# Kernel optimization log

Measured on AMD Instinct MI355X. Metric: run time of the kernel, lower is better.

Reference implementation:

```python
import jax, jax.numpy as jnp
import numpy as np

CHUNK_SIZE = 1024  # module default chunk_size


def setup_inputs() -> dict:
    key = jax.random.key(0)
    kq, kk, kv = jax.random.split(key, 3)
    B, H, S, D = 2, 16, 2048, 64
    q = jax.random.normal(kq, (B, H, S, D), dtype=jnp.float32)
    k = jax.random.normal(kk, (B, H, S, D), dtype=jnp.float32)
    v = jax.random.normal(kv, (B, H, S, D), dtype=jnp.float32)
    return {"q": q, "k": k, "v": v}


def reference(q, k, v):
    # Chunked causal attention: q split into chunks of CHUNK_SIZE along seq,
    # each chunk attends to the full K/V with causal mask (tril, diagonal=start).
    B, H, S, D = q.shape
    scale = D ** (-0.5)
    cs = CHUNK_SIZE
    nc = S // cs  # S is a multiple of chunk_size here
    qc = q.reshape(B, H, nc, cs, D)
    # scores: [B, H, nc, cs, S]
    scores = jnp.einsum('bhncd,bhsd->bhncs', qc, k) * scale
    # causal mask per chunk: key position j visible iff j <= chunk_start + i
    row = (jnp.arange(nc) * cs)[:, None, None] + jnp.arange(cs)[None, :, None]  # [nc, cs, 1]
    col = jnp.arange(S)[None, None, :]  # [1, 1, S]
    causal = col <= row  # [nc, cs, S]
    scores = jnp.where(causal[None, None], scores, -jnp.inf)
    attn = jax.nn.softmax(scores, axis=-1)
    out = jnp.einsum('bhncs,bhsd->bhncd', attn, v)
    return out.reshape(B, H, S, D)
```

## Files before the change

### kernel.cpp

```cpp
#include <hip/hip_runtime.h>

typedef __bf16 bf16x8 __attribute__((ext_vector_type(8)));
typedef float f32x4 __attribute__((ext_vector_type(4)));

#define S_LEN 2048
#define D_DIM 64
#define NHEAD 32

typedef __attribute__((address_space(1))) const void gas;
typedef __attribute__((address_space(3))) void las;

__global__ __launch_bounds__(256) void convert_kv(const float* __restrict__ K,
                                                  const float* __restrict__ V,
                                                  __bf16* __restrict__ Kb,
                                                  __bf16* __restrict__ Vtg) {
    const int head = blockIdx.y;
    const int s0   = blockIdx.x * 64;
    const int tr   = threadIdx.x >> 2;
    const int tc   = (threadIdx.x & 3) << 4;
    const size_t ib = (size_t)head * (S_LEN * D_DIM) + (size_t)(s0 + tr) * D_DIM + tc;

    __shared__ __bf16 tb[64][72];

    {
        const float* kr = K + ib;
        f32x4 a = *(const f32x4*)kr, b = *(const f32x4*)(kr + 4),
              c = *(const f32x4*)(kr + 8), d = *(const f32x4*)(kr + 12);
        bf16x8 o0, o1;
        #pragma unroll
        for (int e = 0; e < 4; ++e) {
            o0[e] = (__bf16)a[e]; o0[e + 4] = (__bf16)b[e];
            o1[e] = (__bf16)c[e]; o1[e + 4] = (__bf16)d[e];
        }
        __bf16* ko = Kb + ib;
        *(bf16x8*)ko = o0; *(bf16x8*)(ko + 8) = o1;
    }
    {
        const float* vr = V + ib;
        f32x4 a = *(const f32x4*)vr, b = *(const f32x4*)(vr + 4),
              c = *(const f32x4*)(vr + 8), d = *(const f32x4*)(vr + 12);
        #pragma unroll
        for (int e = 0; e < 4; ++e) {
            tb[tc +  e][tr] = (__bf16)a[e];
            tb[tc + 4 + e][tr] = (__bf16)b[e];
            tb[tc + 8 + e][tr] = (__bf16)c[e];
            tb[tc + 12 + e][tr] = (__bf16)d[e];
        }
    }
    __syncthreads();
    {
        bf16x8 o0, o1;
        #pragma unroll
        for (int e = 0; e < 8; ++e) { o0[e] = tb[tr][tc + e]; o1[e] = tb[tr][tc + 8 + e]; }
        __bf16* vo = Vtg + (size_t)head * (D_DIM * S_LEN) + (size_t)tr * S_LEN + s0 + tc;
        *(bf16x8*)vo = o0; *(bf16x8*)(vo + 8) = o1;
    }
}

__global__ __launch_bounds__(256, 4) void attn_fwd(const float* __restrict__ Q,
                                                   const __bf16* __restrict__ Kb,
                                                   const __bf16* __restrict__ Vg,
                                                   float* __restrict__ O) {
    const int b    = blockIdx.x;
    const int xcd  = b & 7;
    const int cs   = (b >> 3) & 31;
    const int j    = b >> 8;
    const int head = xcd * 4 + (cs >> 3);
    const int slot = cs & 7;
    const int chunk = (j == 0) ? slot : (j == 1) ? (31 - slot)
                    : (j == 2) ? (slot + 8) : (23 - slot);

    const int tid  = threadIdx.x;
    const int wave = tid >> 6;
    const int lane = tid & 63;
    const int l15  = lane & 15;
    const int lhi  = lane >> 4;

    const int q0 = chunk * 64 + wave * 16;
    const size_t qbase = (size_t)head * (S_LEN * D_DIM);
    const size_t vbase = (size_t)head * (D_DIM * S_LEN);
    const float qscale = 0.125f * 1.44269504088896340736f;

    __shared__ __align__(16) __bf16 Klds[2][64][64];
    __shared__ __align__(16) __bf16 Vt[2][64][64];
    __shared__ __align__(16) __bf16 Plds[4][16][64];

    const int xsw = (lane & 7) ^ ((lane >> 3) & 7);
    const size_t kOff = (size_t)(lane >> 3) * D_DIM + (size_t)xsw * 8;
    const size_t vOff = (size_t)(lane >> 3) * S_LEN + (size_t)xsw * 8;
    const __bf16* kgw = Kb + qbase + (size_t)(wave * 16) * D_DIM + kOff;
    const __bf16* vgw = Vg + vbase + (size_t)(wave * 16) * S_LEN + vOff;

    bf16x8 qf[2];
    {
        const float* qrow = Q + qbase + (size_t)(q0 + l15) * D_DIM + lhi * 8;
        #pragma unroll
        for (int h = 0; h < 2; ++h) {
            f32x4 a = *(const f32x4*)(qrow + h * 32);
            f32x4 bq = *(const f32x4*)(qrow + h * 32 + 4);
            bf16x8 t;
            #pragma unroll
            for (int e = 0; e < 4; ++e) { t[e] = (__bf16)(a[e] * qscale); t[e + 4] = (__bf16)(bq[e] * qscale); }
            qf[h] = t;
        }
    }

    f32x4 acc[4];
    #pragma unroll
    for (int td = 0; td < 4; ++td) acc[td] = (f32x4){0.f, 0.f, 0.f, 0.f};
    float m_r = -1e30f, l_r = 0.f;

    auto stage = [&](int kv0, int bufi) {
        const __bf16* kg = kgw + (size_t)kv0 * D_DIM;
        const __bf16* vg = vgw + kv0;
        __builtin_amdgcn_global_load_lds((gas*)kg,                 (las*)&Klds[bufi][wave * 16][0],     16, 0, 0);
        __builtin_amdgcn_global_load_lds((gas*)(kg + 8 * D_DIM),   (las*)&Klds[bufi][wave * 16 + 8][0], 16, 0, 0);
        __builtin_amdgcn_global_load_lds((gas*)vg,                 (las*)&Vt[bufi][wave * 16][0],       16, 0, 0);
        __builtin_amdgcn_global_load_lds((gas*)(vg + 8 * S_LEN),   (las*)&Vt[bufi][wave * 16 + 8][0],   16, 0, 0);
    };

    stage(0, 0);

    const int nt = chunk + 1;
    for (int kt = 0; kt < nt; ++kt) {
        const int cur = kt & 1;
        asm volatile("s_waitcnt vmcnt(0)" ::: "memory");
        __syncthreads();

        if (kt + 1 < nt) stage((kt + 1) << 6, cur ^ 1);

        f32x4 s[4];
        #pragma unroll
        for (int ct = 0; ct < 4; ++ct) s[ct] = (f32x4){0.f, 0.f, 0.f, 0.f};
        __builtin_amdgcn_s_setprio(1);
        #pragma unroll
        for (int h = 0; h < 2; ++h) {
            #pragma unroll
            for (int ct = 0; ct < 4; ++ct) {
                const int krow = ct * 16 + l15;
                bf16x8 kf = *(const bf16x8*)&Klds[cur][krow][(h * 32 + lhi * 8) ^ ((l15 & 7) << 3)];
                s[ct] = __builtin_amdgcn_mfma_f32_16x16x32_bf16(kf, qf[h], s[ct], 0, 0, 0);
            }
        }
        __builtin_amdgcn_s_setprio(0);

        if (kt == nt - 1) {
            const int kv0 = kt << 6;
            const int qg = q0 + l15;
            #pragma unroll
            for (int ct = 0; ct < 4; ++ct)
                #pragma unroll
                for (int r = 0; r < 4; ++r) {
                    const int kg = kv0 + ct * 16 + lhi * 4 + r;
                    if (kg > qg) s[ct][r] = -1e30f;
                }
        }

        float mm = fmaxf(fmaxf(fmaxf(s[0][0], s[0][1]), fmaxf(s[0][2], s[0][3])),
                         fmaxf(fmaxf(s[1][0], s[1][1]), fmaxf(s[1][2], s[1][3])));
        mm = fmaxf(mm, fmaxf(fmaxf(fmaxf(s[2][0], s[2][1]), fmaxf(s[2][2], s[2][3])),
                             fmaxf(fmaxf(s[3][0], s[3][1]), fmaxf(s[3][2], s[3][3]))));
        mm = fmaxf(mm, __shfl_xor(mm, 16));
        mm = fmaxf(mm, __shfl_xor(mm, 32));
        if (!__all(mm - m_r <= 8.0f)) {
            const float mn = fmaxf(m_r, mm);
            const float f = exp2f(m_r - mn);
            m_r = mn;
            l_r *= f;
            #pragma unroll
            for (int r = 0; r < 4; ++r) {
                const float fr = __shfl(f, lhi * 4 + r);
                #pragma unroll
                for (int td = 0; td < 4; ++td) acc[td][r] *= fr;
            }
        }
        float ps = 0.f;
        #pragma unroll
        for (int ct = 0; ct < 4; ++ct)
            #pragma unroll
            for (int r = 0; r < 4; ++r) {
                const float p = exp2f(s[ct][r] - m_r);
                s[ct][r] = p;
                ps += p;
            }
        ps += __shfl_xor(ps, 16);
        ps += __shfl_xor(ps, 32);
        l_r += ps;

        #pragma unroll
        for (int ct = 0; ct < 4; ++ct) {
            union { __bf16 h[4]; unsigned long long u; } pw;
            #pragma unroll
            for (int r = 0; r < 4; ++r) pw.h[r] = (__bf16)s[ct][r];
            *(unsigned long long*)&Plds[wave][l15][(ct * 16 + lhi * 4) ^ ((l15 & 7) << 3)] = pw.u;
        }
        asm volatile("s_waitcnt lgkmcnt(0)" ::: "memory");
        bf16x8 pf[2];
        #pragma unroll
        for (int kh = 0; kh < 2; ++kh)
            pf[kh] = *(const bf16x8*)&Plds[wave][l15][(kh * 32 + lhi * 8) ^ ((l15 & 7) << 3)];
        asm volatile("" ::: "memory");

        __builtin_amdgcn_s_setprio(1);
        #pragma unroll
        for (int kh = 0; kh < 2; ++kh) {
            #pragma unroll
            for (int td = 0; td < 4; ++td) {
                const int vrow = td * 16 + l15;
                bf16x8 vf = *(const bf16x8*)&Vt[cur][vrow][(kh * 32 + lhi * 8) ^ ((vrow & 7) << 3)];
                acc[td] = __builtin_amdgcn_mfma_f32_16x16x32_bf16(pf[kh], vf, acc[td], 0, 0, 0);
            }
        }
        __builtin_amdgcn_s_setprio(0);
    }

    float* orow = O + qbase + (size_t)q0 * D_DIM;
    #pragma unroll
    for (int r = 0; r < 4; ++r) {
        const float inv = 1.0f / __shfl(l_r, lhi * 4 + r);
        #pragma unroll
        for (int td = 0; td < 4; ++td)
            orow[(size_t)(lhi * 4 + r) * D_DIM + td * 16 + l15] = acc[td][r] * inv;
    }
}

__global__ __launch_bounds__(256, 4) void attn_fwd_fb(const float* __restrict__ Q,
                                                      const float* __restrict__ K,
                                                      const float* __restrict__ V,
                                                      float* __restrict__ O) {
    const int b    = blockIdx.x;
    const int xcd  = b & 7;
    const int cs   = (b >> 3) & 31;
    const int j    = b >> 8;
    const int head = xcd * 4 + (cs >> 3);
    const int slot = cs & 7;
    const int chunk = (j == 0) ? slot : (j == 1) ? (31 - slot)
                    : (j == 2) ? (slot + 8) : (23 - slot);

    const int tid  = threadIdx.x;
    const int wave = tid >> 6;
    const int lane = tid & 63;
    const int l15  = lane & 15;
    const int lhi  = lane >> 4;

    const int q0 = chunk * 64 + wave * 16;
    const size_t base = (size_t)head * (S_LEN * D_DIM);
    const float qscale = 0.125f * 1.44269504088896340736f;

    __shared__ __align__(16) __bf16 Klds[2][64][64];
    __shared__ __align__(16) __bf16 Vt[2][64][64];
    __shared__ __align__(16) __bf16 Plds[4][16][64];

    const int rk = tid >> 2;
    const int ck = (tid & 3) << 4;
    const int kp = tid & 31;
    const int dc = tid >> 5;
    const int swk = (rk & 7) << 3;

    bf16x8 qf[2];
    {
        const float* qrow = Q + base + (size_t)(q0 + l15) * D_DIM + lhi * 8;
        #pragma unroll
        for (int h = 0; h < 2; ++h) {
            f32x4 a = *(const f32x4*)(qrow + h * 32);
            f32x4 bq = *(const f32x4*)(qrow + h * 32 + 4);
            bf16x8 t;
            #pragma unroll
            for (int e = 0; e < 4; ++e) { t[e] = (__bf16)(a[e] * qscale); t[e + 4] = (__bf16)(bq[e] * qscale); }
            qf[h] = t;
        }
    }

    f32x4 acc[4];
    #pragma unroll
    for (int td = 0; td < 4; ++td) acc[td] = (f32x4){0.f, 0.f, 0.f, 0.f};
    float m_r = -1e30f, l_r = 0.f;

    f32x4 pk[4], pva[2], pvb[2];
    {
        const float* ks = K + base + (size_t)rk * D_DIM + ck;
        #pragma unroll
        for (int i = 0; i < 4; ++i) pk[i] = *(const f32x4*)(ks + 4 * i);
        const float* v0 = V + base + (size_t)(2 * kp) * D_DIM + dc * 8;
        pva[0] = *(const f32x4*)v0;           pva[1] = *(const f32x4*)(v0 + 4);
        pvb[0] = *(const f32x4*)(v0 + D_DIM); pvb[1] = *(const f32x4*)(v0 + D_DIM + 4);
        bf16x8 k0, k1;
        #pragma unroll
        for (int e = 0; e < 4; ++e) {
            k0[e] = (__bf16)pk[0][e]; k0[e + 4] = (__bf16)pk[1][e];
            k1[e] = (__bf16)pk[2][e]; k1[e + 4] = (__bf16)pk[3][e];
        }
        *(bf16x8*)&Klds[0][rk][ck ^ swk] = k0;
        *(bf16x8*)&Klds[0][rk][(ck + 8) ^ swk] = k1;
        #pragma unroll
        for (int jj = 0; jj < 8; ++jj) {
            const int d = dc * 8 + jj;
            const float av = (jj < 4) ? pva[0][jj & 3] : pva[1][jj & 3];
            const float bv = (jj < 4) ? pvb[0][jj & 3] : pvb[1][jj & 3];
            union { __bf16 h[2]; unsigned int u; } t;
            t.h[0] = (__bf16)av; t.h[1] = (__bf16)bv;
            *(unsigned int*)&Vt[0][d][(2 * kp) ^ ((d & 7) << 3)] = t.u;
        }
    }

    const int nt = chunk + 1;
    for (int kt = 0; kt < nt; ++kt) {
        const int cur = kt & 1;
        __syncthreads();
        const bool pre = (kt + 1 < nt);
        if (pre) {
            const int kv1 = (kt + 1) << 6;
            const float* ks = K + base + (size_t)(kv1 + rk) * D_DIM + ck;
            #pragma unroll
            for (int i = 0; i < 4; ++i) pk[i] = *(const f32x4*)(ks + 4 * i);
            const float* v0 = V + base + (size_t)(kv1 + 2 * kp) * D_DIM + dc * 8;
            pva[0] = *(const f32x4*)v0;           pva[1] = *(const f32x4*)(v0 + 4);
            pvb[0] = *(const f32x4*)(v0 + D_DIM); pvb[1] = *(const f32x4*)(v0 + D_DIM + 4);
        }

        f32x4 s[4];
        #pragma unroll
        for (int ct = 0; ct < 4; ++ct) s[ct] = (f32x4){0.f, 0.f, 0.f, 0.f};
        #pragma unroll
        for (int h = 0; h < 2; ++h) {
            #pragma unroll
            for (int ct = 0; ct < 4; ++ct) {
                const int krow = ct * 16 + l15;
                bf16x8 kf = *(const bf16x8*)&Klds[cur][krow][(h * 32 + lhi * 8) ^ ((l15 & 7) << 3)];
                s[ct] = __builtin_amdgcn_mfma_f32_16x16x32_bf16(kf, qf[h], s[ct], 0, 0, 0);
            }
        }

        if (kt == nt - 1) {
            const int kv0 = kt << 6;
            const int qg = q0 + l15;
            #pragma unroll
            for (int ct = 0; ct < 4; ++ct)
                #pragma unroll
                for (int r = 0; r < 4; ++r) {
                    const int kg = kv0 + ct * 16 + lhi * 4 + r;
                    if (kg > qg) s[ct][r] = -1e30f;
                }
        }

        float mm = fmaxf(fmaxf(fmaxf(s[0][0], s[0][1]), fmaxf(s[0][2], s[0][3])),
                         fmaxf(fmaxf(s[1][0], s[1][1]), fmaxf(s[1][2], s[1][3])));
        mm = fmaxf(mm, fmaxf(fmaxf(fmaxf(s[2][0], s[2][1]), fmaxf(s[2][2], s[2][3])),
                             fmaxf(fmaxf(s[3][0], s[3][1]), fmaxf(s[3][2], s[3][3]))));
        mm = fmaxf(mm, __shfl_xor(mm, 16));
        mm = fmaxf(mm, __shfl_xor(mm, 32));
        if (!__all(mm - m_r <= 8.0f)) {
            const float mn = fmaxf(m_r, mm);
            const float f = exp2f(m_r - mn);
            m_r = mn;
            l_r *= f;
            #pragma unroll
            for (int r = 0; r < 4; ++r) {
                const float fr = __shfl(f, lhi * 4 + r);
                #pragma unroll
                for (int td = 0; td < 4; ++td) acc[td][r] *= fr;
            }
        }
        float ps = 0.f;
        #pragma unroll
        for (int ct = 0; ct < 4; ++ct)
            #pragma unroll
            for (int r = 0; r < 4; ++r) {
                const float p = exp2f(s[ct][r] - m_r);
                s[ct][r] = p;
                ps += p;
            }
        ps += __shfl_xor(ps, 16);
        ps += __shfl_xor(ps, 32);
        l_r += ps;

        #pragma unroll
        for (int ct = 0; ct < 4; ++ct) {
            union { __bf16 h[4]; unsigned long long u; } pw;
            #pragma unroll
            for (int r = 0; r < 4; ++r) pw.h[r] = (__bf16)s[ct][r];
            *(unsigned long long*)&Plds[wave][l15][(ct * 16 + lhi * 4) ^ ((l15 & 7) << 3)] = pw.u;
        }
        asm volatile("s_waitcnt lgkmcnt(0)" ::: "memory");
        bf16x8 pf[2];
        #pragma unroll
        for (int kh = 0; kh < 2; ++kh)
            pf[kh] = *(const bf16x8*)&Plds[wave][l15][(kh * 32 + lhi * 8) ^ ((l15 & 7) << 3)];
        asm volatile("" ::: "memory");

        #pragma unroll
        for (int kh = 0; kh < 2; ++kh) {
            #pragma unroll
            for (int td = 0; td < 4; ++td) {
                const int vrow = td * 16 + l15;
                bf16x8 vf = *(const bf16x8*)&Vt[cur][vrow][(kh * 32 + lhi * 8) ^ ((vrow & 7) << 3)];
                acc[td] = __builtin_amdgcn_mfma_f32_16x16x32_bf16(pf[kh], vf, acc[td], 0, 0, 0);
            }
        }

        if (pre) {
            const int nxt = cur ^ 1;
            bf16x8 k0, k1;
            #pragma unroll
            for (int e = 0; e < 4; ++e) {
                k0[e] = (__bf16)pk[0][e]; k0[e + 4] = (__bf16)pk[1][e];
                k1[e] = (__bf16)pk[2][e]; k1[e + 4] = (__bf16)pk[3][e];
            }
            *(bf16x8*)&Klds[nxt][rk][ck ^ swk] = k0;
            *(bf16x8*)&Klds[nxt][rk][(ck + 8) ^ swk] = k1;
            #pragma unroll
            for (int jj = 0; jj < 8; ++jj) {
                const int d = dc * 8 + jj;
                const float av = (jj < 4) ? pva[0][jj & 3] : pva[1][jj & 3];
                const float bv = (jj < 4) ? pvb[0][jj & 3] : pvb[1][jj & 3];
                union { __bf16 h[2]; unsigned int u; } t;
                t.h[0] = (__bf16)av; t.h[1] = (__bf16)bv;
                *(unsigned int*)&Vt[nxt][d][(2 * kp) ^ ((d & 7) << 3)] = t.u;
            }
        }
    }

    float* orow = O + base + (size_t)q0 * D_DIM;
    #pragma unroll
    for (int r = 0; r < 4; ++r) {
        const float inv = 1.0f / __shfl(l_r, lhi * 4 + r);
        #pragma unroll
        for (int td = 0; td < 4; ++td)
            orow[(size_t)(lhi * 4 + r) * D_DIM + td * 16 + l15] = acc[td][r] * inv;
    }
}

extern "C" void kernel_launch(void* const* d_in, const int* in_sizes, int n_in,
                              void* d_out, int out_size, void* d_ws, size_t ws_size,
                              hipStream_t stream) {
    const float* q = (const float*)d_in[0];
    const float* k = (const float*)d_in[1];
    const float* v = (const float*)d_in[2];
    float* o = (float*)d_out;
    const size_t elems = (size_t)NHEAD * S_LEN * D_DIM;
    if (ws_size >= 2 * elems * sizeof(__bf16)) {
        __bf16* Kb  = (__bf16*)d_ws;
        __bf16* Vtg = Kb + elems;
        convert_kv<<<dim3(32, 32), dim3(256), 0, stream>>>(k, v, Kb, Vtg);
        attn_fwd<<<dim3(1024), dim3(256), 0, stream>>>(q, Kb, Vtg, o);
    } else {
        attn_fwd_fb<<<dim3(1024), dim3(256), 0, stream>>>(q, k, v, o);
    }
}
```

Measured before the change: 62.21 us.

## Pair causal query chunks per block to balance work across a halved grid

Each block now processes two query chunks, cA and 31-cA, back to back in one fused loop of 33 KV tiles. This gives every block the same amount of work and halves the grid to 512 blocks. It writes the first chunk's output mid-loop, then resets the softmax state and switches the Q fragments. The aim is to remove tail imbalance from causal triangular work and per-block startup cost, at the price of fewer blocks in flight and longer-running blocks.

```diff
diff --git a/kernel.cpp b/kernel.cpp
--- a/kernel.cpp
+++ b/kernel.cpp
@@ -66,9 +66,9 @@
     const int cs   = (b >> 3) & 31;
     const int j    = b >> 8;
     const int head = xcd * 4 + (cs >> 3);
-    const int slot = cs & 7;
-    const int chunk = (j == 0) ? slot : (j == 1) ? (31 - slot)
-                    : (j == 2) ? (slot + 8) : (23 - slot);
+    const int pr   = (cs & 7) + (j << 3);
+    const int cA   = pr;
+    const int cB   = 31 - pr;
 
     const int tid  = threadIdx.x;
     const int wave = tid >> 6;
@@ -76,7 +76,6 @@
     const int l15  = lane & 15;
     const int lhi  = lane >> 4;
 
-    const int q0 = chunk * 64 + wave * 16;
     const size_t qbase = (size_t)head * (S_LEN * D_DIM);
     const size_t vbase = (size_t)head * (D_DIM * S_LEN);
     const float qscale = 0.125f * 1.44269504088896340736f;
@@ -91,8 +90,12 @@
     const __bf16* kgw = Kb + qbase + (size_t)(wave * 16) * D_DIM + kOff;
     const __bf16* vgw = Vg + vbase + (size_t)(wave * 16) * S_LEN + vOff;
 
-    bf16x8 qf[2];
-    {
+    const int q0A = cA * 64 + wave * 16;
+    const int q0B = cB * 64 + wave * 16;
+    bf16x8 qfA[2], qfB[2];
+    #pragma unroll
+    for (int ph = 0; ph < 2; ++ph) {
+        const int q0 = ph ? q0B : q0A;
         const float* qrow = Q + qbase + (size_t)(q0 + l15) * D_DIM + lhi * 8;
         #pragma unroll
         for (int h = 0; h < 2; ++h) {
@@ -101,7 +104,7 @@
             bf16x8 t;
             #pragma unroll
             for (int e = 0; e < 4; ++e) { t[e] = (__bf16)(a[e] * qscale); t[e + 4] = (__bf16)(bq[e] * qscale); }
-            qf[h] = t;
+            if (ph) qfB[h] = t; else qfA[h] = t;
         }
     }
 
@@ -109,6 +112,9 @@
     #pragma unroll
     for (int td = 0; td < 4; ++td) acc[td] = (f32x4){0.f, 0.f, 0.f, 0.f};
     float m_r = -1e30f, l_r = 0.f;
+
+    bf16x8 qcur[2] = {qfA[0], qfA[1]};
+    int q0cur = q0A;
 
     auto stage = [&](int kv0, int bufi) {
         const __bf16* kg = kgw + (size_t)kv0 * D_DIM;
@@ -119,15 +125,31 @@
         __builtin_amdgcn_global_load_lds((gas*)(vg + 8 * S_LEN),   (las*)&Vt[bufi][wave * 16 + 8][0],   16, 0, 0);
     };
 
+    auto write_out = [&](int q0) {
+        float* orow = O + qbase + (size_t)q0 * D_DIM;
+        #pragma unroll
+        for (int r = 0; r < 4; ++r) {
+            const float inv = 1.0f / __shfl(l_r, lhi * 4 + r);
+            #pragma unroll
+            for (int td = 0; td < 4; ++td)
+                orow[(size_t)(lhi * 4 + r) * D_DIM + td * 16 + l15] = acc[td][r] * inv;
+        }
+    };
+
     stage(0, 0);
 
-    const int nt = chunk + 1;
-    for (int kt = 0; kt < nt; ++kt) {
-        const int cur = kt & 1;
+    const int NT = 33;
+    for (int t = 0; t < NT; ++t) {
+        const int cur = t & 1;
         asm volatile("s_waitcnt vmcnt(0)" ::: "memory");
         __syncthreads();
 
-        if (kt + 1 < nt) stage((kt + 1) << 6, cur ^ 1);
+        if (t + 1 < NT) {
+            const int t1 = t + 1;
+            const int kvn = ((t1 <= cA) ? t1 : (t1 - cA - 1)) << 6;
+            stage(kvn, cur ^ 1);
+        }
+        const int kv0 = ((t <= cA) ? t : (t - cA - 1)) << 6;
 
         f32x4 s[4];
         #pragma unroll
@@ -139,14 +161,13 @@
             for (int ct = 0; ct < 4; ++ct) {
                 const int krow = ct * 16 + l15;
                 bf16x8 kf = *(const bf16x8*)&Klds[cur][krow][(h * 32 + lhi * 8) ^ ((l15 & 7) << 3)];
-                s[ct] = __builtin_amdgcn_mfma_f32_16x16x32_bf16(kf, qf[h], s[ct], 0, 0, 0);
+                s[ct] = __builtin_amdgcn_mfma_f32_16x16x32_bf16(kf, qcur[h], s[ct], 0, 0, 0);
             }
         }
         __builtin_amdgcn_s_setprio(0);
 
-        if (kt == nt - 1) {
-            const int kv0 = kt << 6;
-            const int qg = q0 + l15;
+        if (t == cA || t == NT - 1) {
+            const int qg = q0cur + l15;
             #pragma unroll
             for (int ct = 0; ct < 4; ++ct)
                 #pragma unroll
@@ -212,16 +233,18 @@
             }
         }
         __builtin_amdgcn_s_setprio(0);
-    }
-
-    float* orow = O + qbase + (size_t)q0 * D_DIM;
-    #pragma unroll
-    for (int r = 0; r < 4; ++r) {
-        const float inv = 1.0f / __shfl(l_r, lhi * 4 + r);
-        #pragma unroll
-        for (int td = 0; td < 4; ++td)
-            orow[(size_t)(lhi * 4 + r) * D_DIM + td * 16 + l15] = acc[td][r] * inv;
-    }
+
+        if (t == cA) {
+            write_out(q0A);
+            #pragma unroll
+            for (int td = 0; td < 4; ++td) acc[td] = (f32x4){0.f, 0.f, 0.f, 0.f};
+            m_r = -1e30f; l_r = 0.f;
+            qcur[0] = qfB[0]; qcur[1] = qfB[1];
+            q0cur = q0B;
+        }
+    }
+
+    write_out(q0B);
 }
 
 __global__ __launch_bounds__(256, 4) void attn_fwd_fb(const float* __restrict__ Q,
@@ -442,7 +465,7 @@
         __bf16* Kb  = (__bf16*)d_ws;
         __bf16* Vtg = Kb + elems;
         convert_kv<<<dim3(32, 32), dim3(256), 0, stream>>>(k, v, Kb, Vtg);
-        attn_fwd<<<dim3(1024), dim3(256), 0, stream>>>(q, Kb, Vtg, o);
+        attn_fwd<<<dim3(512), dim3(256), 0, stream>>>(q, Kb, Vtg, o);
     } else {
         attn_fwd_fb<<<dim3(1024), dim3(256), 0, stream>>>(q, k, v, o);
     }
```

Result: slower. 67.98 us (+9.3%).

## Replace double-buffered LDS direct loads with register prefetch and single LDS buffer

Applied to the files above, without the earlier changes.

The attention kernel stops using global_load_lds into double-buffered K/V shared tiles. It now prefetches the next K/V tile into registers, writes it to a single swizzled LDS buffer each iteration, and adds a second barrier. Halving LDS lets launch bounds rise from 4 to 6 blocks per SM for more occupancy, at the cost of extra registers, an extra __syncthreads per tile, and explicit LDS stores.

```diff
diff --git a/kernel.cpp b/kernel.cpp
--- a/kernel.cpp
+++ b/kernel.cpp
@@ -6,9 +6,6 @@
 #define S_LEN 2048
 #define D_DIM 64
 #define NHEAD 32
-
-typedef __attribute__((address_space(1))) const void gas;
-typedef __attribute__((address_space(3))) void las;
 
 __global__ __launch_bounds__(256) void convert_kv(const float* __restrict__ K,
                                                   const float* __restrict__ V,
@@ -57,7 +54,7 @@
     }
 }
 
-__global__ __launch_bounds__(256, 4) void attn_fwd(const float* __restrict__ Q,
+__global__ __launch_bounds__(256, 6) void attn_fwd(const float* __restrict__ Q,
                                                    const __bf16* __restrict__ Kb,
                                                    const __bf16* __restrict__ Vg,
                                                    float* __restrict__ O) {
@@ -81,15 +78,16 @@
     const size_t vbase = (size_t)head * (D_DIM * S_LEN);
     const float qscale = 0.125f * 1.44269504088896340736f;
 
-    __shared__ __align__(16) __bf16 Klds[2][64][64];
-    __shared__ __align__(16) __bf16 Vt[2][64][64];
+    __shared__ __align__(16) __bf16 Klds[64][64];
+    __shared__ __align__(16) __bf16 Vt[64][64];
     __shared__ __align__(16) __bf16 Plds[4][16][64];
 
-    const int xsw = (lane & 7) ^ ((lane >> 3) & 7);
-    const size_t kOff = (size_t)(lane >> 3) * D_DIM + (size_t)xsw * 8;
-    const size_t vOff = (size_t)(lane >> 3) * S_LEN + (size_t)xsw * 8;
-    const __bf16* kgw = Kb + qbase + (size_t)(wave * 16) * D_DIM + kOff;
-    const __bf16* vgw = Vg + vbase + (size_t)(wave * 16) * S_LEN + vOff;
+    const int sr  = tid >> 2;
+    const int su0 = (tid & 3) << 1;
+    const int sw0 = (su0 ^ (sr & 7)) << 3;
+    const int sw1 = ((su0 + 1) ^ (sr & 7)) << 3;
+    const __bf16* kSrc = Kb + qbase + (size_t)sr * D_DIM + su0 * 8;
+    const __bf16* vSrc = Vg + vbase + (size_t)sr * S_LEN + su0 * 8;
 
     bf16x8 qf[2];
     {
@@ -110,24 +108,28 @@
     for (int td = 0; td < 4; ++td) acc[td] = (f32x4){0.f, 0.f, 0.f, 0.f};
     float m_r = -1e30f, l_r = 0.f;
 
-    auto stage = [&](int kv0, int bufi) {
-        const __bf16* kg = kgw + (size_t)kv0 * D_DIM;
-        const __bf16* vg = vgw + kv0;
-        __builtin_amdgcn_global_load_lds((gas*)kg,                 (las*)&Klds[bufi][wave * 16][0],     16, 0, 0);
-        __builtin_amdgcn_global_load_lds((gas*)(kg + 8 * D_DIM),   (las*)&Klds[bufi][wave * 16 + 8][0], 16, 0, 0);
-        __builtin_amdgcn_global_load_lds((gas*)vg,                 (las*)&Vt[bufi][wave * 16][0],       16, 0, 0);
-        __builtin_amdgcn_global_load_lds((gas*)(vg + 8 * S_LEN),   (las*)&Vt[bufi][wave * 16 + 8][0],   16, 0, 0);
-    };
-
-    stage(0, 0);
+    bf16x8 pK0, pK1, pV0, pV1;
+    pK0 = *(const bf16x8*)kSrc;  pK1 = *(const bf16x8*)(kSrc + 8);
+    pV0 = *(const bf16x8*)vSrc;  pV1 = *(const bf16x8*)(vSrc + 8);
 
     const int nt = chunk + 1;
     for (int kt = 0; kt < nt; ++kt) {
-        const int cur = kt & 1;
-        asm volatile("s_waitcnt vmcnt(0)" ::: "memory");
         __syncthreads();
 
-        if (kt + 1 < nt) stage((kt + 1) << 6, cur ^ 1);
+        *(bf16x8*)&Klds[sr][sw0] = pK0;
+        *(bf16x8*)&Klds[sr][sw1] = pK1;
+        *(bf16x8*)&Vt[sr][sw0]   = pV0;
+        *(bf16x8*)&Vt[sr][sw1]   = pV1;
+
+        if (kt + 1 < nt) {
+            const int kv1 = (kt + 1) << 6;
+            const __bf16* kg = kSrc + (size_t)kv1 * D_DIM;
+            const __bf16* vg = vSrc + kv1;
+            pK0 = *(const bf16x8*)kg;  pK1 = *(const bf16x8*)(kg + 8);
+            pV0 = *(const bf16x8*)vg;  pV1 = *(const bf16x8*)(vg + 8);
+        }
+
+        __syncthreads();
 
         f32x4 s[4];
         #pragma unroll
@@ -138,7 +140,7 @@
             #pragma unroll
             for (int ct = 0; ct < 4; ++ct) {
                 const int krow = ct * 16 + l15;
-                bf16x8 kf = *(const bf16x8*)&Klds[cur][krow][(h * 32 + lhi * 8) ^ ((l15 & 7) << 3)];
+                bf16x8 kf = *(const bf16x8*)&Klds[krow][(h * 32 + lhi * 8) ^ ((l15 & 7) << 3)];
                 s[ct] = __builtin_amdgcn_mfma_f32_16x16x32_bf16(kf, qf[h], s[ct], 0, 0, 0);
             }
         }
@@ -207,7 +209,7 @@
             #pragma unroll
             for (int td = 0; td < 4; ++td) {
                 const int vrow = td * 16 + l15;
-                bf16x8 vf = *(const bf16x8*)&Vt[cur][vrow][(kh * 32 + lhi * 8) ^ ((vrow & 7) << 3)];
+                bf16x8 vf = *(const bf16x8*)&Vt[vrow][(kh * 32 + lhi * 8) ^ ((vrow & 7) << 3)];
                 acc[td] = __builtin_amdgcn_mfma_f32_16x16x32_bf16(pf[kh], vf, acc[td], 0, 0, 0);
             }
         }
```

Result: slower. 71.11 us (+14.3%).

## Split long causal query chunks across two KV ranges and merge partials

Applied to the files above, without the earlier changes.

Query chunks 16-31 now have their KV range split into two jobs, listed in a static table sorted by work so that block lengths are balanced across 1536 blocks. Each split job writes its unnormalized accumulator plus running max and sum to workspace, and a new combine kernel merges the two halves with log-sum-exp weighting. This targets the tail imbalance of causal attention, where long chunks dominate. The cost is an extra kernel launch and the partial-result traffic through global memory.

```diff
diff --git a/kernel.cpp b/kernel.cpp
--- a/kernel.cpp
+++ b/kernel.cpp
@@ -9,6 +9,21 @@
 
 typedef __attribute__((address_space(1))) const void gas;
 typedef __attribute__((address_space(3))) void las;
+
+#define J(c, t0, nt) ((unsigned short)((c) | ((t0) << 5) | ((nt) << 10)))
+__device__ const unsigned short JOBS[48] = {
+    J(15,0,16), J(30,0,16), J(31,0,16), J(31,16,16),
+    J(14,0,15), J(28,0,15), J(29,0,15), J(29,15,15), J(30,16,15),
+    J(13,0,14), J(26,0,14), J(27,0,14), J(27,14,14), J(28,15,14),
+    J(12,0,13), J(24,0,13), J(25,0,13), J(25,13,13), J(26,14,13),
+    J(11,0,12), J(22,0,12), J(23,0,12), J(23,12,12), J(24,13,12),
+    J(10,0,11), J(20,0,11), J(21,0,11), J(21,11,11), J(22,12,11),
+    J( 9,0,10), J(18,0,10), J(19,0,10), J(19,10,10), J(20,11,10),
+    J( 8,0, 9), J(16,0, 9), J(17,0, 9), J(17, 9, 9), J(18,10, 9),
+    J( 7,0, 8), J(16,9, 8),
+    J( 6,0, 7), J( 5,0, 6), J( 4,0, 5), J( 3,0, 4), J( 2,0, 3), J( 1,0, 2), J( 0,0, 1)
+};
+#define PART_FLOATS 4224
 
 __global__ __launch_bounds__(256) void convert_kv(const float* __restrict__ K,
                                                   const float* __restrict__ V,
@@ -57,18 +72,32 @@
     }
 }
 
+template <int SPLIT>
 __global__ __launch_bounds__(256, 4) void attn_fwd(const float* __restrict__ Q,
                                                    const __bf16* __restrict__ Kb,
                                                    const __bf16* __restrict__ Vg,
-                                                   float* __restrict__ O) {
-    const int b    = blockIdx.x;
-    const int xcd  = b & 7;
-    const int cs   = (b >> 3) & 31;
-    const int j    = b >> 8;
-    const int head = xcd * 4 + (cs >> 3);
-    const int slot = cs & 7;
-    const int chunk = (j == 0) ? slot : (j == 1) ? (31 - slot)
-                    : (j == 2) ? (slot + 8) : (23 - slot);
+                                                   float* __restrict__ O,
+                                                   float* __restrict__ Ppart) {
+    int head, chunk, t0, nt;
+    if constexpr (SPLIT) {
+        const int b   = blockIdx.x;
+        const int xcd = b & 7;
+        const int w   = b >> 3;
+        head = xcd * 4 + (w & 3);
+        const unsigned short jj = JOBS[w >> 2];
+        chunk = jj & 31; t0 = (jj >> 5) & 31; nt = jj >> 10;
+    } else {
+        const int b    = blockIdx.x;
+        const int xcd  = b & 7;
+        const int cs   = (b >> 3) & 31;
+        const int j    = b >> 8;
+        head = xcd * 4 + (cs >> 3);
+        const int slot = cs & 7;
+        chunk = (j == 0) ? slot : (j == 1) ? (31 - slot)
+              : (j == 2) ? (slot + 8) : (23 - slot);
+        t0 = 0; nt = chunk + 1;
+    }
+    const bool diagJob = (t0 + nt - 1 == chunk);
 
     const int tid  = threadIdx.x;
     const int wave = tid >> 6;
@@ -113,21 +142,21 @@
     auto stage = [&](int kv0, int bufi) {
         const __bf16* kg = kgw + (size_t)kv0 * D_DIM;
         const __bf16* vg = vgw + kv0;
-        __builtin_amdgcn_global_load_lds((gas*)kg,                 (las*)&Klds[bufi][wave * 16][0],     16, 0, 0);
-        __builtin_amdgcn_global_load_lds((gas*)(kg + 8 * D_DIM),   (las*)&Klds[bufi][wave * 16 + 8][0], 16, 0, 0);
-        __builtin_amdgcn_global_load_lds((gas*)vg,                 (las*)&Vt[bufi][wave * 16][0],       16, 0, 0);
-        __builtin_amdgcn_global_load_lds((gas*)(vg + 8 * S_LEN),   (las*)&Vt[bufi][wave * 16 + 8][0],   16, 0, 0);
+        __builtin_amdgcn_global_load_lds((gas*)kg,               (las*)&Klds[bufi][wave * 16][0],     16, 0, 0);
+        __builtin_amdgcn_global_load_lds((gas*)(kg + 8 * D_DIM), (las*)&Klds[bufi][wave * 16 + 8][0], 16, 0, 0);
+        __builtin_amdgcn_global_load_lds((gas*)vg,               (las*)&Vt[bufi][wave * 16][0],       16, 0, 0);
+        __builtin_amdgcn_global_load_lds((gas*)(vg + 8 * S_LEN), (las*)&Vt[bufi][wave * 16 + 8][0],   16, 0, 0);
     };
 
-    stage(0, 0);
-
-    const int nt = chunk + 1;
+    stage(t0 << 6, 0);
+
     for (int kt = 0; kt < nt; ++kt) {
         const int cur = kt & 1;
         asm volatile("s_waitcnt vmcnt(0)" ::: "memory");
         __syncthreads();
 
-        if (kt + 1 < nt) stage((kt + 1) << 6, cur ^ 1);
+        if (kt + 1 < nt) stage((t0 + kt + 1) << 6, cur ^ 1);
+        const int kv0 = (t0 + kt) << 6;
 
         f32x4 s[4];
         #pragma unroll
@@ -144,8 +173,7 @@
         }
         __builtin_amdgcn_s_setprio(0);
 
-        if (kt == nt - 1) {
-            const int kv0 = kt << 6;
+        if (diagJob && kt == nt - 1) {
             const int qg = q0 + l15;
             #pragma unroll
             for (int ct = 0; ct < 4; ++ct)
@@ -214,13 +242,56 @@
         __builtin_amdgcn_s_setprio(0);
     }
 
-    float* orow = O + qbase + (size_t)q0 * D_DIM;
+    if (!SPLIT || chunk < 16) {
+        float* orow = O + qbase + (size_t)q0 * D_DIM;
+        #pragma unroll
+        for (int r = 0; r < 4; ++r) {
+            const float inv = 1.0f / __shfl(l_r, lhi * 4 + r);
+            #pragma unroll
+            for (int td = 0; td < 4; ++td)
+                orow[(size_t)(lhi * 4 + r) * D_DIM + td * 16 + l15] = acc[td][r] * inv;
+        }
+    } else {
+        const int seg = (t0 != 0) ? 1 : 0;
+        float* pp = Ppart + (size_t)(head * 32 + (chunk - 16) * 2 + seg) * PART_FLOATS;
+        if (lhi == 0) {
+            pp[wave * 16 + l15] = m_r;
+            pp[64 + wave * 16 + l15] = l_r;
+        }
+        #pragma unroll
+        for (int r = 0; r < 4; ++r)
+            #pragma unroll
+            for (int td = 0; td < 4; ++td)
+                pp[128 + (size_t)(wave * 16 + lhi * 4 + r) * 64 + td * 16 + l15] = acc[td][r];
+    }
+}
+
+__global__ __launch_bounds__(256) void combine(const float* __restrict__ Ppart,
+                                               float* __restrict__ O) {
+    const int head = blockIdx.y;
+    const int ch   = blockIdx.x;
+    const float* PA = Ppart + (size_t)(head * 32 + ch * 2) * PART_FLOATS;
+    const float* PB = PA + PART_FLOATS;
+    const int row = threadIdx.x >> 2;
+    const int c0  = (threadIdx.x & 3) << 4;
+
+    const float mA = PA[row], lA = PA[64 + row];
+    const float mB = PB[row], lB = PB[64 + row];
+    const float M  = fmaxf(mA, mB);
+    const float wA = exp2f(mA - M), wB = exp2f(mB - M);
+    const float inv = 1.0f / (lA * wA + lB * wB);
+
+    const float* a = PA + 128 + (size_t)row * 64 + c0;
+    const float* b = PB + 128 + (size_t)row * 64 + c0;
+    float* o = O + (size_t)head * (S_LEN * D_DIM) + (size_t)((16 + ch) * 64 + row) * D_DIM + c0;
     #pragma unroll
-    for (int r = 0; r < 4; ++r) {
-        const float inv = 1.0f / __shfl(l_r, lhi * 4 + r);
-        #pragma unroll
-        for (int td = 0; td < 4; ++td)
-            orow[(size_t)(lhi * 4 + r) * D_DIM + td * 16 + l15] = acc[td][r] * inv;
+    for (int i = 0; i < 4; ++i) {
+        f32x4 va = *(const f32x4*)(a + 4 * i);
+        f32x4 vb = *(const f32x4*)(b + 4 * i);
+        f32x4 vo;
+        #pragma unroll
+        for (int e = 0; e < 4; ++e) vo[e] = (va[e] * wA + vb[e] * wB) * inv;
+        *(f32x4*)(o + 4 * i) = vo;
     }
 }
 
@@ -438,11 +509,20 @@
     const float* v = (const float*)d_in[2];
     float* o = (float*)d_out;
     const size_t elems = (size_t)NHEAD * S_LEN * D_DIM;
-    if (ws_size >= 2 * elems * sizeof(__bf16)) {
+    const size_t kvBytes = 2 * elems * sizeof(__bf16);
+    const size_t partBytes = (size_t)NHEAD * 32 * PART_FLOATS * sizeof(float);
+    if (ws_size >= kvBytes + partBytes) {
+        __bf16* Kb  = (__bf16*)d_ws;
+        __bf16* Vtg = Kb + elems;
+        float* Pp   = (float*)((char*)d_ws + kvBytes);
+        convert_kv<<<dim3(32, 32), dim3(256), 0, stream>>>(k, v, Kb, Vtg);
+        attn_fwd<1><<<dim3(1536), dim3(256), 0, stream>>>(q, Kb, Vtg, o, Pp);
+        combine<<<dim3(16, 32), dim3(256), 0, stream>>>(Pp, o);
+    } else if (ws_size >= kvBytes) {
         __bf16* Kb  = (__bf16*)d_ws;
         __bf16* Vtg = Kb + elems;
         convert_kv<<<dim3(32, 32), dim3(256), 0, stream>>>(k, v, Kb, Vtg);
-        attn_fwd<<<dim3(1024), dim3(256), 0, stream>>>(q, Kb, Vtg, o);
+        attn_fwd<0><<<dim3(1024), dim3(256), 0, stream>>>(q, Kb, Vtg, o, nullptr);
     } else {
         attn_fwd_fb<<<dim3(1024), dim3(256), 0, stream>>>(q, k, v, o);
     }
```

New measurement: 64.87 us. +4.3%, slower.
